# Kernel tuning notes

Measured on AMD Instinct MI355X. Metric: run time of the kernel, lower is better.

## Reference

```python
import jax, jax.numpy as jnp
import numpy as np

EPSILON = 1e-8
TAU = 0.1

def setup_inputs() -> dict:
    key = jax.random.key(0)
    x = jax.random.normal(key, (8192, 256), dtype=jnp.float32)
    return {"x": x}

def reference(x):
    # L2-normalize rows (torch F.normalize: x / max(||x||, 1e-12))
    norm = jnp.maximum(jnp.linalg.norm(x, axis=1, keepdims=True), 1e-12)
    xn = x / norm
    n = xn.shape[0]
    # pairwise cosine similarity via GEMM (equivalent to broadcast sum in source)
    cos = (xn @ xn.T) / TAU                      # [N, N]
    exp_cos = jnp.exp(cos)
    # zero out diagonal (self-similarity)
    exp_cos = exp_cos * (1.0 - jnp.eye(n, dtype=exp_cos.dtype))
    loss = jnp.log(exp_cos.sum(axis=1) / (n - 1) + EPSILON)
    return jnp.mean(loss)
```

## Files before the change

### kernel.cpp

```cpp
#include <hip/hip_runtime.h>
#include <hip/hip_bf16.h>
#include <math.h>

#define TAU_INV_LOG2E 14.4269504088896340736f
#define EPS 1e-8f

typedef __attribute__((ext_vector_type(8))) short bf16x8;
typedef __attribute__((ext_vector_type(4))) float f32x4;

static __device__ __forceinline__ unsigned short f2bf(float f) {
    unsigned int u = __float_as_uint(f);
    unsigned int r = (u + 0x7fffu + ((u >> 16) & 1u)) >> 16;
    return (unsigned short)r;
}

static __device__ __forceinline__ void glds16(const void* g, void* l) {
    __builtin_amdgcn_global_load_lds(
        (const __attribute__((address_space(1))) unsigned int*)g,
        (__attribute__((address_space(3))) unsigned int*)l,
        16, 0, 0);
}

__global__ __launch_bounds__(256) void normalize_kernel(
    const float* __restrict__ x, unsigned short* __restrict__ xn,
    float* __restrict__ rowsum, int N) {
    const int wave = threadIdx.x >> 6;
    const int lane = threadIdx.x & 63;
    const int row  = blockIdx.x * 4 + wave;
    if (row >= N) return;

    if (threadIdx.x < 4) {
        int rr = blockIdx.x * 4 + threadIdx.x;
        if (rr < N) rowsum[rr] = 0.0f;
    }

    const float4 v = ((const float4*)(x + (size_t)row * 256))[lane];
    float s = v.x * v.x + v.y * v.y + v.z * v.z + v.w * v.w;
    s += __shfl_xor(s, 1);
    s += __shfl_xor(s, 2);
    s += __shfl_xor(s, 4);
    s += __shfl_xor(s, 8);
    s += __shfl_xor(s, 16);
    s += __shfl_xor(s, 32);
    const float norm = fmaxf(sqrtf(s), 1e-12f);
    const float rinv = 1.0f / norm;

    ushort4 o;
    o.x = f2bf(v.x * rinv);
    o.y = f2bf(v.y * rinv);
    o.z = f2bf(v.z * rinv);
    o.w = f2bf(v.w * rinv);
    ((ushort4*)(xn + (size_t)row * 256))[lane] = o;
}

__global__ __launch_bounds__(256, 3) void gemm_exp_rowsum_kernel(
    const unsigned short* __restrict__ xn, float* __restrict__ rowsum, int N) {
    const int D = 256;
    __shared__ unsigned short As[128 * 64];
    __shared__ unsigned short Bs[128 * 64];

    const int tid   = threadIdx.x;
    const int wave  = tid >> 6;
    const int lane  = tid & 63;
    const int waveM = wave >> 1;
    const int waveN = wave & 1;
    const int quad  = lane >> 4;
    const int l16   = lane & 15;

    const int B = N >> 7;
    const int t = blockIdx.x;
    int bi = (int)((2.0 * B + 1.0 -
                    sqrt((2.0 * B + 1.0) * (2.0 * B + 1.0) - 8.0 * (double)t)) * 0.5);
    while (bi > 0 && t < bi * B - (bi * (bi - 1)) / 2) --bi;
    while (t >= (bi + 1) * B - ((bi + 1) * bi) / 2) ++bi;
    const int bj = bi + (t - (bi * B - (bi * (bi - 1)) / 2));
    const bool diag = (bi == bj);

    const int iBase = bi * 128;
    const int jBase = bj * 128;

    f32x4 acc[4][4];
    #pragma unroll
    for (int mt = 0; mt < 4; ++mt)
        #pragma unroll
        for (int nt = 0; nt < 4; ++nt)
            acc[mt][nt] = (f32x4){0.f, 0.f, 0.f, 0.f};

    const int lrow = lane >> 3;
    const int lsw  = (lane & 7) ^ lrow;

    for (int k0 = 0; k0 < D; k0 += 64) {
        #pragma unroll
        for (int it = 0; it < 4; ++it) {
            const int q   = wave * 4 + it;
            const int row = q * 8 + lrow;
            glds16(xn + (size_t)(iBase + row) * D + k0 + lsw * 8, As + q * 512);
            if (!diag)
                glds16(xn + (size_t)(jBase + row) * D + k0 + lsw * 8, Bs + q * 512);
        }
        __syncthreads();

        const unsigned short* Bp = diag ? As : Bs;
        #pragma unroll
        for (int kk = 0; kk < 64; kk += 32) {
            bf16x8 a[4], b[4];
            const int cA = (kk >> 3) + quad;
            #pragma unroll
            for (int tt = 0; tt < 4; ++tt) {
                const int rA = waveM * 64 + tt * 16 + l16;
                a[tt] = *(const bf16x8*)(As + (rA >> 3) * 512 + (rA & 7) * 64 +
                                          ((cA ^ (rA & 7)) * 8));
                const int rB = waveN * 64 + tt * 16 + l16;
                b[tt] = *(const bf16x8*)(Bp + (rB >> 3) * 512 + (rB & 7) * 64 +
                                          ((cA ^ (rB & 7)) * 8));
            }
            #pragma unroll
            for (int mt = 0; mt < 4; ++mt)
                #pragma unroll
                for (int nt = 0; nt < 4; ++nt)
                    acc[mt][nt] = __builtin_amdgcn_mfma_f32_16x16x32_bf16(
                        a[mt], b[nt], acc[mt][nt], 0, 0, 0);
        }
        __syncthreads();
    }

    float rsum[4][4];
    float csum[4] = {0.f, 0.f, 0.f, 0.f};
    #pragma unroll
    for (int mt = 0; mt < 4; ++mt)
        #pragma unroll
        for (int r = 0; r < 4; ++r) rsum[mt][r] = 0.f;

    #pragma unroll
    for (int mt = 0; mt < 4; ++mt) {
        const int gi0 = iBase + waveM * 64 + mt * 16 + quad * 4;
        #pragma unroll
        for (int nt = 0; nt < 4; ++nt) {
            const int gj = jBase + waveN * 64 + nt * 16 + l16;
            #pragma unroll
            for (int r = 0; r < 4; ++r) {
                float e = __builtin_amdgcn_exp2f(acc[mt][nt][r] * TAU_INV_LOG2E);
                if (gi0 + r == gj) e = 0.0f;
                rsum[mt][r] += e;
                csum[nt] += e;
            }
        }
    }
    #pragma unroll
    for (int mt = 0; mt < 4; ++mt) {
        const int gi0 = iBase + waveM * 64 + mt * 16 + quad * 4;
        #pragma unroll
        for (int r = 0; r < 4; ++r) {
            float s = rsum[mt][r];
            s += __shfl_xor(s, 1);
            s += __shfl_xor(s, 2);
            s += __shfl_xor(s, 4);
            s += __shfl_xor(s, 8);
            if (l16 == 0) atomicAdd(&rowsum[gi0 + r], s);
        }
    }
    if (!diag) {
        #pragma unroll
        for (int nt = 0; nt < 4; ++nt) {
            float s = csum[nt];
            s += __shfl_xor(s, 16);
            s += __shfl_xor(s, 32);
            if (quad == 0)
                atomicAdd(&rowsum[jBase + waveN * 64 + nt * 16 + l16], s);
        }
    }
}

__global__ __launch_bounds__(256) void finalize_kernel(
    const float* __restrict__ rowsum, float* __restrict__ out, int N) {
    __shared__ float red[4];
    const float inv = 1.0f / (float)(N - 1);
    float acc = 0.f;
    for (int i = threadIdx.x; i < N; i += 256)
        acc += logf(rowsum[i] * inv + EPS);
    acc += __shfl_xor(acc, 1);
    acc += __shfl_xor(acc, 2);
    acc += __shfl_xor(acc, 4);
    acc += __shfl_xor(acc, 8);
    acc += __shfl_xor(acc, 16);
    acc += __shfl_xor(acc, 32);
    const int wave = threadIdx.x >> 6;
    const int lane = threadIdx.x & 63;
    if (lane == 0) red[wave] = acc;
    __syncthreads();
    if (threadIdx.x == 0) {
        float total = red[0] + red[1] + red[2] + red[3];
        out[0] = total / (float)N;
    }
}

extern "C" void kernel_launch(void* const* d_in, const int* in_sizes, int n_in,
                              void* d_out, int out_size, void* d_ws, size_t ws_size,
                              hipStream_t stream) {
    const float* x = (const float*)d_in[0];
    const int D = 256;
    const int N = in_sizes[0] / D;

    unsigned short* xn = (unsigned short*)d_ws;
    float* rowsum = (float*)((char*)d_ws + (size_t)N * D * sizeof(unsigned short));
    float* out = (float*)d_out;

    normalize_kernel<<<(N + 3) / 4, 256, 0, stream>>>(x, xn, rowsum, N);

    const int B = N / 128;
    const int T = B * (B + 1) / 2;
    gemm_exp_rowsum_kernel<<<T, 256, 0, stream>>>(xn, rowsum, N);

    finalize_kernel<<<1, 256, 0, stream>>>(rowsum, out, N);
}
```

Baseline: 108.7 us.

## Load GEMM operands directly from global into registers, drop LDS staging

The GEMM kernel no longer stages A/B tiles through shared memory with global_load_lds and barriers. Each lane loads its bf16x8 MFMA fragments straight from global memory (served by L2/L1), with the K loop fully unrolled over 8 steps. This removes the LDS traffic and __syncthreads, but each row fragment is now fetched redundantly by several waves and the loads are less coalesced. The finalize kernel is also widened from 256 to 1024 threads.

```diff
diff --git a/kernel.cpp b/kernel.cpp
--- a/kernel.cpp
+++ b/kernel.cpp
@@ -12,13 +12,6 @@
     unsigned int u = __float_as_uint(f);
     unsigned int r = (u + 0x7fffu + ((u >> 16) & 1u)) >> 16;
     return (unsigned short)r;
-}
-
-static __device__ __forceinline__ void glds16(const void* g, void* l) {
-    __builtin_amdgcn_global_load_lds(
-        (const __attribute__((address_space(1))) unsigned int*)g,
-        (__attribute__((address_space(3))) unsigned int*)l,
-        16, 0, 0);
 }
 
 __global__ __launch_bounds__(256) void normalize_kernel(
@@ -56,8 +49,6 @@
 __global__ __launch_bounds__(256, 3) void gemm_exp_rowsum_kernel(
     const unsigned short* __restrict__ xn, float* __restrict__ rowsum, int N) {
     const int D = 256;
-    __shared__ unsigned short As[128 * 64];
-    __shared__ unsigned short Bs[128 * 64];
 
     const int tid   = threadIdx.x;
     const int wave  = tid >> 6;
@@ -79,6 +70,14 @@
     const int iBase = bi * 128;
     const int jBase = bj * 128;
 
+    const unsigned short* Ap[4];
+    const unsigned short* Bp[4];
+    #pragma unroll
+    for (int tt = 0; tt < 4; ++tt) {
+        Ap[tt] = xn + (size_t)(iBase + waveM * 64 + tt * 16 + l16) * D + quad * 8;
+        Bp[tt] = xn + (size_t)(jBase + waveN * 64 + tt * 16 + l16) * D + quad * 8;
+    }
+
     f32x4 acc[4][4];
     #pragma unroll
     for (int mt = 0; mt < 4; ++mt)
@@ -86,42 +85,20 @@
         for (int nt = 0; nt < 4; ++nt)
             acc[mt][nt] = (f32x4){0.f, 0.f, 0.f, 0.f};
 
-    const int lrow = lane >> 3;
-    const int lsw  = (lane & 7) ^ lrow;
-
-    for (int k0 = 0; k0 < D; k0 += 64) {
+    #pragma unroll
+    for (int ks = 0; ks < 8; ++ks) {
+        bf16x8 a[4], b[4];
         #pragma unroll
-        for (int it = 0; it < 4; ++it) {
-            const int q   = wave * 4 + it;
-            const int row = q * 8 + lrow;
-            glds16(xn + (size_t)(iBase + row) * D + k0 + lsw * 8, As + q * 512);
-            if (!diag)
-                glds16(xn + (size_t)(jBase + row) * D + k0 + lsw * 8, Bs + q * 512);
+        for (int tt = 0; tt < 4; ++tt) {
+            a[tt] = *(const bf16x8*)(Ap[tt] + ks * 32);
+            b[tt] = *(const bf16x8*)(Bp[tt] + ks * 32);
         }
-        __syncthreads();
-
-        const unsigned short* Bp = diag ? As : Bs;
         #pragma unroll
-        for (int kk = 0; kk < 64; kk += 32) {
-            bf16x8 a[4], b[4];
-            const int cA = (kk >> 3) + quad;
+        for (int mt = 0; mt < 4; ++mt)
             #pragma unroll
-            for (int tt = 0; tt < 4; ++tt) {
-                const int rA = waveM * 64 + tt * 16 + l16;
-                a[tt] = *(const bf16x8*)(As + (rA >> 3) * 512 + (rA & 7) * 64 +
-                                          ((cA ^ (rA & 7)) * 8));
-                const int rB = waveN * 64 + tt * 16 + l16;
-                b[tt] = *(const bf16x8*)(Bp + (rB >> 3) * 512 + (rB & 7) * 64 +
-                                          ((cA ^ (rB & 7)) * 8));
-            }
-            #pragma unroll
-            for (int mt = 0; mt < 4; ++mt)
-                #pragma unroll
-                for (int nt = 0; nt < 4; ++nt)
-                    acc[mt][nt] = __builtin_amdgcn_mfma_f32_16x16x32_bf16(
-                        a[mt], b[nt], acc[mt][nt], 0, 0, 0);
-        }
-        __syncthreads();
+            for (int nt = 0; nt < 4; ++nt)
+                acc[mt][nt] = __builtin_amdgcn_mfma_f32_16x16x32_bf16(
+                    a[mt], b[nt], acc[mt][nt], 0, 0, 0);
     }
 
     float rsum[4][4];
@@ -171,12 +148,12 @@
     }
 }
 
-__global__ __launch_bounds__(256) void finalize_kernel(
+__global__ __launch_bounds__(1024) void finalize_kernel(
     const float* __restrict__ rowsum, float* __restrict__ out, int N) {
-    __shared__ float red[4];
+    __shared__ float red[16];
     const float inv = 1.0f / (float)(N - 1);
     float acc = 0.f;
-    for (int i = threadIdx.x; i < N; i += 256)
+    for (int i = threadIdx.x; i < N; i += 1024)
         acc += logf(rowsum[i] * inv + EPS);
     acc += __shfl_xor(acc, 1);
     acc += __shfl_xor(acc, 2);
@@ -189,7 +166,9 @@
     if (lane == 0) red[wave] = acc;
     __syncthreads();
     if (threadIdx.x == 0) {
-        float total = red[0] + red[1] + red[2] + red[3];
+        float total = 0.f;
+        #pragma unroll
+        for (int w = 0; w < 16; ++w) total += red[w];
         out[0] = total / (float)N;
     }
 }
@@ -211,5 +190,5 @@
     const int T = B * (B + 1) / 2;
     gemm_exp_rowsum_kernel<<<T, 256, 0, stream>>>(xn, rowsum, N);
 
-    finalize_kernel<<<1, 256, 0, stream>>>(rowsum, out, N);
+    finalize_kernel<<<1, 1024, 0, stream>>>(rowsum, out, N);
 }
```

New measurement: 144.8 us. 1.33x slower.

## Widen GEMM tile to 128x256 and fuse finalize via last-block ticket

Applied to the files above, without the earlier changes.

The GEMM block now computes a 128x256 strip (two 128x128 column tiles, one per pair of waves) over the upper triangle, with each wave holding an 8x4 MFMA accumulator grid. The A tile is shared across both column tiles, which raises operand reuse per LDS load and halves the block count. Tiles below the diagonal are masked out in the strip. The separate finalize kernel is removed: the last block to finish, found with an atomic ticket counter, computes the log-mean, saving one launch. In exchange, register pressure rises (occupancy hint drops to 2), some waves sit idle on diagonal strips, and the grid size and triangle mapping are hardcoded for N=8192.

```diff
diff --git a/kernel.cpp b/kernel.cpp
--- a/kernel.cpp
+++ b/kernel.cpp
@@ -1,6 +1,5 @@
 #include <hip/hip_runtime.h>
 #include <hip/hip_bf16.h>
-#include <math.h>
 
 #define TAU_INV_LOG2E 14.4269504088896340736f
 #define EPS 1e-8f
@@ -23,7 +22,7 @@
 
 __global__ __launch_bounds__(256) void normalize_kernel(
     const float* __restrict__ x, unsigned short* __restrict__ xn,
-    float* __restrict__ rowsum, int N) {
+    float* __restrict__ rowsum, int* __restrict__ done, int N) {
     const int wave = threadIdx.x >> 6;
     const int lane = threadIdx.x & 63;
     const int row  = blockIdx.x * 4 + wave;
@@ -33,6 +32,7 @@
         int rr = blockIdx.x * 4 + threadIdx.x;
         if (rr < N) rowsum[rr] = 0.0f;
     }
+    if (blockIdx.x == 0 && threadIdx.x == 0) *done = 0;
 
     const float4 v = ((const float4*)(x + (size_t)row * 256))[lane];
     float s = v.x * v.x + v.y * v.y + v.z * v.z + v.w * v.w;
@@ -53,144 +53,148 @@
     ((ushort4*)(xn + (size_t)row * 256))[lane] = o;
 }
 
-__global__ __launch_bounds__(256, 3) void gemm_exp_rowsum_kernel(
-    const unsigned short* __restrict__ xn, float* __restrict__ rowsum, int N) {
+__global__ __launch_bounds__(256, 2) void gemm_exp_rowsum_kernel(
+    const unsigned short* __restrict__ xn, float* __restrict__ rowsum,
+    int* __restrict__ done, float* __restrict__ out, int N, int nblocks) {
     const int D = 256;
-    __shared__ unsigned short As[128 * 64];
-    __shared__ unsigned short Bs[128 * 64];
+    __shared__ unsigned short As[16 * 512];
+    __shared__ unsigned short Bs[32 * 512];
+    __shared__ int ticket_s;
+    __shared__ float red[4];
 
     const int tid   = threadIdx.x;
     const int wave  = tid >> 6;
     const int lane  = tid & 63;
-    const int waveM = wave >> 1;
-    const int waveN = wave & 1;
     const int quad  = lane >> 4;
     const int l16   = lane & 15;
 
-    const int B = N >> 7;
-    const int t = blockIdx.x;
-    int bi = (int)((2.0 * B + 1.0 -
-                    sqrt((2.0 * B + 1.0) * (2.0 * B + 1.0) - 8.0 * (double)t)) * 0.5);
-    while (bi > 0 && t < bi * B - (bi * (bi - 1)) / 2) --bi;
-    while (t >= (bi + 1) * B - ((bi + 1) * bi) / 2) ++bi;
-    const int bj = bi + (t - (bi * B - (bi * (bi - 1)) / 2));
-    const bool diag = (bi == bj);
+    int bi = 0, trem = blockIdx.x;
+    while (trem >= 32 - (bi >> 1)) { trem -= 32 - (bi >> 1); ++bi; }
+    const int jp = (bi >> 1) + trem;
 
     const int iBase = bi * 128;
-    const int jBase = bj * 128;
-
-    f32x4 acc[4][4];
+    const int jBase = jp * 256;
+
+    const int myTile = wave >> 1;
+    const int bj     = 2 * jp + myTile;
+    const bool valid = (bj >= bi);
+    const bool colOk = (bj > bi);
+
+    const int lrow = lane >> 3;
+    const int lsw  = (lane & 7) ^ lrow;
+
+    f32x4 acc[8][4];
     #pragma unroll
-    for (int mt = 0; mt < 4; ++mt)
+    for (int mt = 0; mt < 8; ++mt)
         #pragma unroll
         for (int nt = 0; nt < 4; ++nt)
             acc[mt][nt] = (f32x4){0.f, 0.f, 0.f, 0.f};
 
-    const int lrow = lane >> 3;
-    const int lsw  = (lane & 7) ^ lrow;
-
     for (int k0 = 0; k0 < D; k0 += 64) {
         #pragma unroll
-        for (int it = 0; it < 4; ++it) {
-            const int q   = wave * 4 + it;
-            const int row = q * 8 + lrow;
-            glds16(xn + (size_t)(iBase + row) * D + k0 + lsw * 8, As + q * 512);
-            if (!diag)
-                glds16(xn + (size_t)(jBase + row) * D + k0 + lsw * 8, Bs + q * 512);
+        for (int it = 0; it < 12; ++it) {
+            const int ch = wave * 12 + it;
+            if (ch < 16) {
+                glds16(xn + (size_t)(iBase + ch * 8 + lrow) * D + k0 + lsw * 8,
+                       As + ch * 512);
+            } else {
+                const int q = ch - 16;
+                glds16(xn + (size_t)(jBase + q * 8 + lrow) * D + k0 + lsw * 8,
+                       Bs + q * 512);
+            }
         }
         __syncthreads();
 
-        const unsigned short* Bp = diag ? As : Bs;
+        if (valid) {
+            #pragma unroll
+            for (int kh = 0; kh < 2; ++kh) {
+                const int cA = kh * 4 + quad;
+                bf16x8 a[8], b[4];
+                #pragma unroll
+                for (int mt = 0; mt < 8; ++mt) {
+                    const int rA = mt * 16 + l16;
+                    a[mt] = *(const bf16x8*)(As + (rA >> 3) * 512 +
+                                             (rA & 7) * 64 + ((cA ^ (rA & 7)) * 8));
+                }
+                #pragma unroll
+                for (int nt = 0; nt < 4; ++nt) {
+                    const int rB = myTile * 128 + (wave & 1) * 64 + nt * 16 + l16;
+                    b[nt] = *(const bf16x8*)(Bs + (rB >> 3) * 512 +
+                                             (rB & 7) * 64 + ((cA ^ (rB & 7)) * 8));
+                }
+                #pragma unroll
+                for (int mt = 0; mt < 8; ++mt)
+                    #pragma unroll
+                    for (int nt = 0; nt < 4; ++nt)
+                        acc[mt][nt] = __builtin_amdgcn_mfma_f32_16x16x32_bf16(
+                            a[mt], b[nt], acc[mt][nt], 0, 0, 0);
+            }
+        }
+        __syncthreads();
+    }
+
+    if (valid) {
+        const int colBase = jBase + myTile * 128 + (wave & 1) * 64;
+        float csum[4] = {0.f, 0.f, 0.f, 0.f};
         #pragma unroll
-        for (int kk = 0; kk < 64; kk += 32) {
-            bf16x8 a[4], b[4];
-            const int cA = (kk >> 3) + quad;
-            #pragma unroll
-            for (int tt = 0; tt < 4; ++tt) {
-                const int rA = waveM * 64 + tt * 16 + l16;
-                a[tt] = *(const bf16x8*)(As + (rA >> 3) * 512 + (rA & 7) * 64 +
-                                          ((cA ^ (rA & 7)) * 8));
-                const int rB = waveN * 64 + tt * 16 + l16;
-                b[tt] = *(const bf16x8*)(Bp + (rB >> 3) * 512 + (rB & 7) * 64 +
-                                          ((cA ^ (rB & 7)) * 8));
-            }
-            #pragma unroll
-            for (int mt = 0; mt < 4; ++mt)
-                #pragma unroll
-                for (int nt = 0; nt < 4; ++nt)
-                    acc[mt][nt] = __builtin_amdgcn_mfma_f32_16x16x32_bf16(
-                        a[mt], b[nt], acc[mt][nt], 0, 0, 0);
-        }
+        for (int mt = 0; mt < 8; ++mt) {
+            const int gi0 = iBase + mt * 16 + quad * 4;
+            float rs[4] = {0.f, 0.f, 0.f, 0.f};
+            #pragma unroll
+            for (int nt = 0; nt < 4; ++nt) {
+                const int gj = colBase + nt * 16 + l16;
+                #pragma unroll
+                for (int r = 0; r < 4; ++r) {
+                    float e = __builtin_amdgcn_exp2f(acc[mt][nt][r] * TAU_INV_LOG2E);
+                    if (gi0 + r == gj) e = 0.0f;
+                    rs[r] += e;
+                    csum[nt] += e;
+                }
+            }
+            #pragma unroll
+            for (int r = 0; r < 4; ++r) {
+                float s = rs[r];
+                s += __shfl_xor(s, 1);
+                s += __shfl_xor(s, 2);
+                s += __shfl_xor(s, 4);
+                s += __shfl_xor(s, 8);
+                if (l16 == 0) atomicAdd(&rowsum[gi0 + r], s);
+            }
+        }
+        if (colOk) {
+            #pragma unroll
+            for (int nt = 0; nt < 4; ++nt) {
+                float s = csum[nt];
+                s += __shfl_xor(s, 16);
+                s += __shfl_xor(s, 32);
+                if (quad == 0) atomicAdd(&rowsum[colBase + nt * 16 + l16], s);
+            }
+        }
+    }
+
+    __threadfence();
+    if (tid == 0)
+        ticket_s = __hip_atomic_fetch_add(done, 1, __ATOMIC_ACQ_REL,
+                                          __HIP_MEMORY_SCOPE_AGENT);
+    __syncthreads();
+    if (ticket_s == nblocks - 1) {
+        const float inv = 1.0f / (float)(N - 1);
+        float accv = 0.f;
+        for (int i = tid; i < N; i += 256) {
+            float v = __hip_atomic_load(&rowsum[i], __ATOMIC_RELAXED,
+                                        __HIP_MEMORY_SCOPE_AGENT);
+            accv += logf(v * inv + EPS);
+        }
+        accv += __shfl_xor(accv, 1);
+        accv += __shfl_xor(accv, 2);
+        accv += __shfl_xor(accv, 4);
+        accv += __shfl_xor(accv, 8);
+        accv += __shfl_xor(accv, 16);
+        accv += __shfl_xor(accv, 32);
+        if (lane == 0) red[wave] = accv;
         __syncthreads();
-    }
-
-    float rsum[4][4];
-    float csum[4] = {0.f, 0.f, 0.f, 0.f};
-    #pragma unroll
-    for (int mt = 0; mt < 4; ++mt)
-        #pragma unroll
-        for (int r = 0; r < 4; ++r) rsum[mt][r] = 0.f;
-
-    #pragma unroll
-    for (int mt = 0; mt < 4; ++mt) {
-        const int gi0 = iBase + waveM * 64 + mt * 16 + quad * 4;
-        #pragma unroll
-        for (int nt = 0; nt < 4; ++nt) {
-            const int gj = jBase + waveN * 64 + nt * 16 + l16;
-            #pragma unroll
-            for (int r = 0; r < 4; ++r) {
-                float e = __builtin_amdgcn_exp2f(acc[mt][nt][r] * TAU_INV_LOG2E);
-                if (gi0 + r == gj) e = 0.0f;
-                rsum[mt][r] += e;
-                csum[nt] += e;
-            }
-        }
-    }
-    #pragma unroll
-    for (int mt = 0; mt < 4; ++mt) {
-        const int gi0 = iBase + waveM * 64 + mt * 16 + quad * 4;
-        #pragma unroll
-        for (int r = 0; r < 4; ++r) {
-            float s = rsum[mt][r];
-            s += __shfl_xor(s, 1);
-            s += __shfl_xor(s, 2);
-            s += __shfl_xor(s, 4);
-            s += __shfl_xor(s, 8);
-            if (l16 == 0) atomicAdd(&rowsum[gi0 + r], s);
-        }
-    }
-    if (!diag) {
-        #pragma unroll
-        for (int nt = 0; nt < 4; ++nt) {
-            float s = csum[nt];
-            s += __shfl_xor(s, 16);
-            s += __shfl_xor(s, 32);
-            if (quad == 0)
-                atomicAdd(&rowsum[jBase + waveN * 64 + nt * 16 + l16], s);
-        }
-    }
-}
-
-__global__ __launch_bounds__(256) void finalize_kernel(
-    const float* __restrict__ rowsum, float* __restrict__ out, int N) {
-    __shared__ float red[4];
-    const float inv = 1.0f / (float)(N - 1);
-    float acc = 0.f;
-    for (int i = threadIdx.x; i < N; i += 256)
-        acc += logf(rowsum[i] * inv + EPS);
-    acc += __shfl_xor(acc, 1);
-    acc += __shfl_xor(acc, 2);
-    acc += __shfl_xor(acc, 4);
-    acc += __shfl_xor(acc, 8);
-    acc += __shfl_xor(acc, 16);
-    acc += __shfl_xor(acc, 32);
-    const int wave = threadIdx.x >> 6;
-    const int lane = threadIdx.x & 63;
-    if (lane == 0) red[wave] = acc;
-    __syncthreads();
-    if (threadIdx.x == 0) {
-        float total = red[0] + red[1] + red[2] + red[3];
-        out[0] = total / (float)N;
+        if (tid == 0)
+            out[0] = (red[0] + red[1] + red[2] + red[3]) / (float)N;
     }
 }
 
@@ -203,13 +207,13 @@
 
     unsigned short* xn = (unsigned short*)d_ws;
     float* rowsum = (float*)((char*)d_ws + (size_t)N * D * sizeof(unsigned short));
+    int* done = (int*)((char*)d_ws + (size_t)N * D * sizeof(unsigned short) +
+                       (size_t)N * sizeof(float));
     float* out = (float*)d_out;
 
-    normalize_kernel<<<(N + 3) / 4, 256, 0, stream>>>(x, xn, rowsum, N);
-
-    const int B = N / 128;
-    const int T = B * (B + 1) / 2;
-    gemm_exp_rowsum_kernel<<<T, 256, 0, stream>>>(xn, rowsum, N);
-
-    finalize_kernel<<<1, 256, 0, stream>>>(rowsum, out, N);
-}
+    normalize_kernel<<<(N + 3) / 4, 256, 0, stream>>>(x, xn, rowsum, done, N);
+
+    const int nblocks = 1056;
+    gemm_exp_rowsum_kernel<<<nblocks, 256, 0, stream>>>(xn, rowsum, done, out,
+                                                        N, nblocks);
+}
```

After: 186.3 us. 1.71x slower.
